# Optimization experiments

Measured on AMD Instinct MI355X. Metric: run time of the kernel, lower is better.

The kernel has to match this reference:

```python
import jax, jax.numpy as jnp
import numpy as np

B, L, D, H = 2, 2048, 1024, 16
DH = D // H
SCALE = DH ** -0.5


def setup_inputs() -> dict:
    key = jax.random.key(0)
    k1, k2, k3 = jax.random.split(key, 3)
    x = jax.random.normal(k1, (B, L, D), dtype=jnp.float32)
    W_qkv = jax.random.normal(k2, (D, 3 * D), dtype=jnp.float32) * 0.02
    b_qkv = jnp.zeros((3 * D,), dtype=jnp.float32)
    W_proj = jax.random.normal(k3, (D, D), dtype=jnp.float32) * 0.02
    b_proj = jnp.zeros((D,), dtype=jnp.float32)
    return {"x": x, "W_qkv": W_qkv, "b_qkv": b_qkv, "W_proj": W_proj, "b_proj": b_proj}


def reference(x, W_qkv, b_qkv, W_proj, b_proj):
    b, l, d = x.shape
    # QKV projection: [B,L,3D] -> [3,B,H,L,DH] matching 'b n (three h d) -> three b h n d'
    qkv = (x @ W_qkv + b_qkv).reshape(b, l, 3, H, DH).transpose(2, 0, 3, 1, 4)
    q, k, v = qkv[0], qkv[1], qkv[2]
    # Causal scores. Chunking in the original is purely a scheduling detail;
    # masks are indexed by absolute row positions, so full attention is identical.
    scores = jnp.einsum('bhqd,bhkd->bhqk', q, k) * SCALE
    mask = jnp.triu(jnp.ones((l, l), dtype=bool), 1)  # True above diagonal
    neg_inf = jnp.finfo(scores.dtype).min
    scores = jnp.where(mask, neg_inf, scores)
    m = jnp.max(scores, axis=-1, keepdims=True)
    e = jnp.where(mask, 0.0, jnp.exp(scores - m))
    attn = e / (jnp.sum(e, axis=-1, keepdims=True) + 1e-6)
    out = jnp.einsum('bhqk,bhkd->bhqd', attn, v)  # [B,H,L,DH]
    out = out.transpose(0, 2, 1, 3).reshape(b, l, d)  # 'b h n d -> b n (h d)'
    return out @ W_proj + b_proj
```

## Files before the change

### kernel.cpp

```cpp
#include <hip/hip_runtime.h>


typedef __bf16 bf16x8 __attribute__((ext_vector_type(8)));
typedef float  f32x4  __attribute__((ext_vector_type(4)));
typedef unsigned short bhalf;
typedef unsigned int   uint32;

#define B_  2
#define L_  2048
#define D_  1024
#define H_  16
#define DH_ 64

#define GPTR(p) ((const __attribute__((address_space(1))) void*)(p))
#define SPTR(p) ((__attribute__((address_space(3))) void*)(p))

static __device__ __forceinline__ float bf2f(bhalf u) {
    union { uint32 u; float f; } x; x.u = ((uint32)u) << 16; return x.f;
}
static __device__ __forceinline__ bhalf f2bf(float f) {
    union { float f; uint32 u; } x; x.f = f;
    uint32 r = x.u + 0x7FFFu + ((x.u >> 16) & 1u);
    return (bhalf)(r >> 16);
}

__global__ void detect_dtype(const uint32* __restrict__ xw, int* __restrict__ flag) {
    int t = threadIdx.x;
    uint32 w = xw[t];
    uint32 e = (w >> 7) & 0xFFu;
    int g = (e < 0x6Fu || e > 0x84u) ? 1 : 0;
#pragma unroll
    for (int off = 32; off; off >>= 1) g += __shfl_xor(g, off);
    if (t == 0) *flag = (g > 16) ? 0 : 1;
}

__global__ void conv_bf16(const void* __restrict__ in, bhalf* __restrict__ out,
                          int n4, const int* __restrict__ flag) {
    const bool isb = (*flag != 0);
    for (int i = blockIdx.x * blockDim.x + threadIdx.x; i < n4;
         i += gridDim.x * blockDim.x) {
        if (isb) {
            ((uint2*)out)[i] = ((const uint2*)in)[i];
        } else {
            float4 v = ((const float4*)in)[i];
            uint2 o;
            o.x = (uint32)f2bf(v.x) | ((uint32)f2bf(v.y) << 16);
            o.y = (uint32)f2bf(v.z) | ((uint32)f2bf(v.w) << 16);
            ((uint2*)out)[i] = o;
        }
    }
}

__global__ void tr_conv(const void* __restrict__ in, bhalf* __restrict__ out,
                        int R, int C, const int* __restrict__ flag) {
    __shared__ bhalf t[32][33];
    const bool isb = (*flag != 0);
    int bx = blockIdx.x, by = blockIdx.y;
    int tx = threadIdx.x, ty = threadIdx.y;
#pragma unroll
    for (int i = 0; i < 32; i += 8) {
        size_t idx = (size_t)(by * 32 + ty + i) * C + bx * 32 + tx;
        t[ty + i][tx] = isb ? ((const bhalf*)in)[idx]
                            : f2bf(((const float*)in)[idx]);
    }
    __syncthreads();
#pragma unroll
    for (int i = 0; i < 32; i += 8)
        out[(size_t)(bx * 32 + ty + i) * R + by * 32 + tx] = t[tx][ty + i];
}


#define GSTAGE(BUF, KK) do {                                                  \
    int kko = (KK);                                                           \
    _Pragma("unroll")                                                         \
    for (int r = 0; r < 2; r++) {                                             \
        int c = r * 256 + tid;                                                \
        int row = c >> 2, p = c & 3;                                          \
        int gch = (p - row - (row >> 2)) & 3;                                 \
        __builtin_amdgcn_global_load_lds(                                     \
            GPTR(a0 + (size_t)row * K + kko + gch * 8),                       \
            SPTR(As[BUF] + (r * 256 + w * 64) * 8), 16, 0, 0);                \
        __builtin_amdgcn_global_load_lds(                                     \
            GPTR(b0 + (size_t)row * K + kko + gch * 8),                       \
            SPTR(Bs[BUF] + (r * 256 + w * 64) * 8), 16, 0, 0);                \
    }                                                                         \
} while (0)

template <int MODE>
__global__ __launch_bounds__(256) void gemm_bt(
        const bhalf* __restrict__ A, const bhalf* __restrict__ Bt,
        const void* __restrict__ bias,
        void* __restrict__ C0, bhalf* __restrict__ Qb,
        bhalf* __restrict__ Kb, bhalf* __restrict__ Vtb,
        int M, int N, int K, const int* __restrict__ flag) {
    __shared__ bhalf As[2][128 * 32];
    __shared__ bhalf Bs[2][128 * 32];
    const bool isb = (*flag != 0);
    const int tid  = threadIdx.x;
    const int w    = tid >> 6, lane = tid & 63;
    const int g    = lane >> 4, cl = lane & 15;
    const int m0   = blockIdx.y * 128, n0 = blockIdx.x * 128;
    const int wr   = (w >> 1) * 64, wc = (w & 1) * 64;

    f32x4 acc[4][4] = {};

    const bhalf* a0 = A  + (size_t)m0 * K;
    const bhalf* b0 = Bt + (size_t)n0 * K;

    GSTAGE(0, 0);
    __syncthreads();

    const int nk = K >> 5;
    for (int t = 0; t < nk; ++t) {
        int cur = t & 1;
        if (t + 1 < nk) GSTAGE(cur ^ 1, (t + 1) << 5);

        bf16x8 af[4], bf4[4];
#pragma unroll
        for (int i = 0; i < 4; i++) {
            int ra = wr + i * 16 + cl;
            af[i]  = *(const bf16x8*)(As[cur] + ra * 32 +
                                      (((g + ra + (ra >> 2)) & 3) * 8));
            int rb = wc + i * 16 + cl;
            bf4[i] = *(const bf16x8*)(Bs[cur] + rb * 32 +
                                      (((g + rb + (rb >> 2)) & 3) * 8));
        }
        __builtin_amdgcn_s_setprio(1);
#pragma unroll
        for (int i = 0; i < 4; i++)
#pragma unroll
            for (int j = 0; j < 4; j++)
                acc[i][j] = __builtin_amdgcn_mfma_f32_16x16x32_bf16(
                    af[i], bf4[j], acc[i][j], 0, 0, 0);
        __builtin_amdgcn_s_setprio(0);

        __syncthreads();
    }

#pragma unroll
    for (int i = 0; i < 4; i++) {
#pragma unroll
        for (int j = 0; j < 4; j++) {
            int nn = n0 + wc + j * 16 + cl;
            float bv = isb ? bf2f(((const bhalf*)bias)[nn])
                           : ((const float*)bias)[nn];
#pragma unroll
            for (int r = 0; r < 4; r++) {
                int mm = m0 + wr + i * 16 + g * 4 + r;
                float v = acc[i][j][r] + bv;
                if (MODE == 0) {
                    if (isb) ((bhalf*)C0)[(size_t)mm * N + nn] = f2bf(v);
                    else     ((float*)C0)[(size_t)mm * N + nn] = v;
                } else {
                    int b = mm >> 11, l = mm & 2047;
                    int three = nn >> 10, rem = nn & 1023;
                    int h = rem >> 6, dh = rem & 63;
                    size_t bh = (size_t)(b * 16 + h);
                    if (three == 0) {
                        Qb[(bh * 2048 + l) * 64 + dh] = f2bf(v * 0.18033688f);
                    } else if (three == 1) {
                        Kb [(bh * 2048 + l) * 64 + dh] = f2bf(v);
                    } else {
                        Vtb[(bh * 64 + dh) * 2048 + l] = f2bf(v);
                    }
                }
            }
        }
    }
}


#define STAGE(BUF, KT) do {                                                   \
    int ktv = (KT);                                                           \
    _Pragma("unroll")                                                         \
    for (int r = 0; r < 4; r++) {                                             \
        int c = r * 256 + tid;                                                \
        int row = c >> 3, p = c & 7;                                          \
        int fsw = (row & 3) | (((row >> 3) & 1) << 2);                        \
        __builtin_amdgcn_global_load_lds(                                     \
            GPTR(Kp + (size_t)(ktv * 128 + row) * 64 + (p ^ fsw) * 8),        \
            SPTR(Ks[BUF] + (r * 256 + w * 64) * 8), 16, 0, 0);                \
    }                                                                         \
    _Pragma("unroll")                                                         \
    for (int r = 0; r < 4; r++) {                                             \
        int c = r * 256 + tid;                                                \
        int row = c >> 4, p = c & 15;                                         \
        __builtin_amdgcn_global_load_lds(                                     \
            GPTR(Vt + (size_t)row * L_ + ktv * 128 + (p ^ (row & 15)) * 8),   \
            SPTR(Vs[BUF] + (r * 256 + w * 64) * 8), 16, 0, 0);                \
    }                                                                         \
} while (0)

#define ATTN_TILE(BUF, KT, QF, QLANE, MVAR, LVAR, OACC, MASK) do {            \
    f32x4 p8[8] = {};                                                         \
    _Pragma("unroll")                                                         \
    for (int s = 0; s < 2; s++) {                                             \
        bf16x8 kf[8];                                                         \
        _Pragma("unroll")                                                     \
        for (int j = 0; j < 8; j++) {                                         \
            int row = (j >> 1) * 32 + (cl >> 2) * 8 + (j & 1) * 4 + (cl & 3); \
            int fsw = (row & 3) | (((row >> 3) & 1) << 2);                    \
            int ch = s * 4 + g;                                               \
            kf[j] = *(const bf16x8*)(Ks[BUF] + row * 64 + ((ch ^ fsw) * 8));  \
        }                                                                     \
        __builtin_amdgcn_s_setprio(1);                                        \
        _Pragma("unroll")                                                     \
        for (int j = 0; j < 8; j++)                                           \
            p8[j] = __builtin_amdgcn_mfma_f32_16x16x32_bf16(                  \
                kf[j], QF[s], p8[j], 0, 0, 0);                                \
        __builtin_amdgcn_s_setprio(0);                                        \
    }                                                                         \
    float mx0 = -__builtin_inff(), mx1 = -__builtin_inff();                   \
    float mx2 = -__builtin_inff(), mx3 = -__builtin_inff();                   \
    _Pragma("unroll")                                                         \
    for (int j = 0; j < 8; j++) {                                             \
        float v0 = p8[j][0], v1 = p8[j][1], v2 = p8[j][2], v3 = p8[j][3];     \
        if (MASK) {                                                           \
            int ka = (KT) * 128 + (j >> 1) * 32 + g * 8 + ((j & 1) << 2);     \
            v0 = (ka + 0 > (QLANE)) ? -__builtin_inff() : v0;                 \
            v1 = (ka + 1 > (QLANE)) ? -__builtin_inff() : v1;                 \
            v2 = (ka + 2 > (QLANE)) ? -__builtin_inff() : v2;                 \
            v3 = (ka + 3 > (QLANE)) ? -__builtin_inff() : v3;                 \
            p8[j][0] = v0; p8[j][1] = v1; p8[j][2] = v2; p8[j][3] = v3;       \
        }                                                                     \
        mx0 = fmaxf(mx0, v0); mx1 = fmaxf(mx1, v1);                           \
        mx2 = fmaxf(mx2, v2); mx3 = fmaxf(mx3, v3);                           \
    }                                                                         \
    float mx = fmaxf(fmaxf(mx0, mx1), fmaxf(mx2, mx3));                       \
    mx = fmaxf(mx, __shfl_xor(mx, 16));                                       \
    mx = fmaxf(mx, __shfl_xor(mx, 32));                                       \
    if (!__all(mx - MVAR <= 8.f)) {       \
        float mnew = fmaxf(MVAR, mx);                                         \
        float alpha = __builtin_amdgcn_exp2f(MVAR - mnew);                    \
        MVAR = mnew;                                                          \
        LVAR *= alpha;                                                        \
        _Pragma("unroll")                                                     \
        for (int r = 0; r < 4; r++) {                                         \
            float ar = __shfl(alpha, g * 4 + r);                              \
            _Pragma("unroll")                                                 \
            for (int dj = 0; dj < 4; dj++) OACC[dj][r] *= ar;                 \
        }                                                                     \
    }                                                                         \
    float s0 = 0.f, s1 = 0.f, s2 = 0.f, s3 = 0.f;                             \
    _Pragma("unroll")                                                         \
    for (int j = 0; j < 8; j++) {                                             \
        float e0 = __builtin_amdgcn_exp2f(p8[j][0] - MVAR);                   \
        float e1 = __builtin_amdgcn_exp2f(p8[j][1] - MVAR);                   \
        float e2 = __builtin_amdgcn_exp2f(p8[j][2] - MVAR);                   \
        float e3 = __builtin_amdgcn_exp2f(p8[j][3] - MVAR);                   \
        p8[j][0] = e0; p8[j][1] = e1; p8[j][2] = e2; p8[j][3] = e3;           \
        s0 += e0; s1 += e1; s2 += e2; s3 += e3;                               \
    }                                                                         \
    float ls = (s0 + s1) + (s2 + s3);                                         \
    ls += __shfl_xor(ls, 16);                                                 \
    ls += __shfl_xor(ls, 32);                                                 \
    LVAR += ls;                                                               \
    _Pragma("unroll")                                                         \
    for (int ks = 0; ks < 4; ks++) {                                          \
        bf16x8 pf;                                                            \
        _Pragma("unroll")                                                     \
        for (int e = 0; e < 8; e++)                                           \
            pf[e] = (__bf16)p8[2 * ks + (e >> 2)][e & 3];                     \
        bf16x8 vf[4];                                                         \
        _Pragma("unroll")                                                     \
        for (int dj = 0; dj < 4; dj++) {                                      \
            int vrow = dj * 16 + cl;                                          \
            int ch = ks * 4 + g;                                              \
            vf[dj] = *(const bf16x8*)(Vs[BUF] + vrow * 128 + ((ch ^ (vrow & 15)) * 8)); \
        }                                                                     \
        __builtin_amdgcn_s_setprio(1);                                        \
        _Pragma("unroll")                                                     \
        for (int dj = 0; dj < 4; dj++)                                        \
            OACC[dj] = __builtin_amdgcn_mfma_f32_16x16x32_bf16(               \
                pf, vf[dj], OACC[dj], 0, 0, 0);                               \
        __builtin_amdgcn_s_setprio(0);                                        \
    }                                                                         \
} while (0)

__global__ __launch_bounds__(256, 2) void attn_fwd(
        const bhalf* __restrict__ Qb, const bhalf* __restrict__ Kb,
        const bhalf* __restrict__ Vtb, bhalf* __restrict__ Ob) {
    __shared__ bhalf Ks[2][128 * 64];
    __shared__ bhalf Vs[2][64 * 128];

    const int bid  = blockIdx.x;
    const int xcd  = bid & 7, slot = bid >> 3;
    const int bx   = slot & 15;
    const int bh   = xcd + 8 * (slot >> 4);
    const int qbA  = 31 - bx;
    const int qbB  = bx;

    const int tid = threadIdx.x;
    const int w = tid >> 6, lane = tid & 63;
    const int g = lane >> 4, cl = lane & 15;

    const bhalf* Q  = Qb  + (size_t)bh * L_ * DH_;
    const bhalf* Kp = Kb  + (size_t)bh * L_ * DH_;
    const bhalf* Vt = Vtb + (size_t)bh * DH_ * L_;

    const int q0A = qbA * 64 + w * 16, qlA = q0A + cl;
    const int q0B = qbB * 64 + w * 16, qlB = q0B + cl;

    bf16x8 qfA[2], qfB[2];
#pragma unroll
    for (int s = 0; s < 2; s++) {
        qfA[s] = *(const bf16x8*)(Q + (size_t)(q0A + cl) * 64 + s * 32 + g * 8);
        qfB[s] = *(const bf16x8*)(Q + (size_t)(q0B + cl) * 64 + s * 32 + g * 8);
    }

    f32x4 oA[4] = {}, oB[4] = {};
    float mA = -__builtin_inff(), lA = 0.f;
    float mB = -__builtin_inff(), lB = 0.f;

    const int nktA = (qbA >> 1) + 1;
    const int nktB = (qbB >> 1) + 1;

    STAGE(0, 0);
    __syncthreads();

    for (int kt = 0; kt < nktA; ++kt) {
        int cur = kt & 1;
        if (kt + 1 < nktA) STAGE(cur ^ 1, kt + 1);
        if (kt < nktB) {
            ATTN_TILE(cur, kt, qfB, qlB, mB, lB, oB, (kt == nktB - 1));
        }
        ATTN_TILE(cur, kt, qfA, qlA, mA, lA, oA, (kt == nktA - 1));
        __syncthreads();
    }

    const int b = bh >> 4, h = bh & 15;
#pragma unroll
    for (int r = 0; r < 4; r++) {
        float lrA = __shfl(lA, g * 4 + r);
        float lrB = __shfl(lB, g * 4 + r);
        float invA = 1.f / (lrA + 1e-6f);
        float invB = 1.f / (lrB + 1e-6f);
        int qrA = q0A + g * 4 + r, qrB = q0B + g * 4 + r;
#pragma unroll
        for (int dj = 0; dj < 4; dj++) {
            Ob[((size_t)b * L_ + qrA) * D_ + h * 64 + dj * 16 + cl] =
                f2bf(oA[dj][r] * invA);
            Ob[((size_t)b * L_ + qrB) * D_ + h * 64 + dj * 16 + cl] =
                f2bf(oB[dj][r] * invB);
        }
    }
}

extern "C" void kernel_launch(void* const* d_in, const int* in_sizes, int n_in,
                              void* d_out, int out_size, void* d_ws, size_t ws_size,
                              hipStream_t stream) {
    const void* x     = d_in[0];
    const void* Wqkv  = d_in[1];
    const void* bqkv  = d_in[2];
    const void* Wproj = d_in[3];
    const void* bproj = d_in[4];

    char* ws = (char*)d_ws;
    const size_t SZ_FLG = 256;
    const size_t SZ_WQT = (size_t)3 * D_ * D_ * 2;
    const size_t SZ_WPT = (size_t)D_ * D_ * 2;
    const size_t SZ_X   = (size_t)B_ * L_ * D_ * 2;
    const size_t SZ_BUF = (size_t)B_ * H_ * L_ * DH_ * 2;

    int*   flag = (int*)ws;
    bhalf* Wq_t = (bhalf*)(ws + SZ_FLG);
    bhalf* Wp_t = (bhalf*)(ws + SZ_FLG + SZ_WQT);
    bhalf* Xb   = (bhalf*)(ws + SZ_FLG + SZ_WQT + SZ_WPT);
    bhalf* Qbuf = (bhalf*)(ws + SZ_FLG + SZ_WQT + SZ_WPT + SZ_X);
    bhalf* Kbuf = (bhalf*)(ws + SZ_FLG + SZ_WQT + SZ_WPT + SZ_X + SZ_BUF);
    bhalf* Vtbf = (bhalf*)(ws + SZ_FLG + SZ_WQT + SZ_WPT + SZ_X + 2 * SZ_BUF);
    bhalf* Obuf = (bhalf*)(ws + SZ_FLG + SZ_WQT + SZ_WPT + SZ_X + 3 * SZ_BUF);

    const int M = B_ * L_;

    detect_dtype<<<1, 64, 0, stream>>>((const uint32*)x, flag);

    conv_bf16<<<2048, 256, 0, stream>>>(x, Xb, (B_ * L_ * D_) / 4, flag);
    tr_conv<<<dim3(3 * D_ / 32, D_ / 32), dim3(32, 8), 0, stream>>>(
        Wqkv, Wq_t, D_, 3 * D_, flag);
    tr_conv<<<dim3(D_ / 32, D_ / 32), dim3(32, 8), 0, stream>>>(
        Wproj, Wp_t, D_, D_, flag);

    gemm_bt<1><<<dim3(3 * D_ / 128, M / 128), 256, 0, stream>>>(
        Xb, Wq_t, bqkv, nullptr, Qbuf, Kbuf, Vtbf, M, 3 * D_, D_, flag);

    attn_fwd<<<dim3(512), 256, 0, stream>>>(Qbuf, Kbuf, Vtbf, Obuf);

    gemm_bt<0><<<dim3(D_ / 128, M / 128), 256, 0, stream>>>(
        Obuf, Wp_t, bproj, d_out, nullptr, nullptr, nullptr, M, D_, D_, flag);
}
```

Before: 125.0 us.

## Triple-buffer GEMM LDS staging and register-stage K/V prefetch in attention

The GEMM moves from double to triple buffering of its LDS tiles. It waits with an explicit vmcnt and uses a single barrier per iteration, so loads run two tiles ahead. The attention kernel drops its double-buffered direct global-to-LDS loads. It now prefetches the next K/V tile into registers and writes them to a single LDS buffer after compute, which halves attention LDS use but adds registers and an extra barrier per tile. In the GEMM, the redundant clamped reload of the last tile on the final iterations and the hand-placed waitcnt both depend on the compiler emitting exactly the expected number of outstanding loads.

```diff
diff --git a/kernel.cpp b/kernel.cpp
--- a/kernel.cpp
+++ b/kernel.cpp
@@ -72,6 +72,7 @@
 
 #define GSTAGE(BUF, KK) do {                                                  \
     int kko = (KK);                                                           \
+    int bufv = (BUF);                                                         \
     _Pragma("unroll")                                                         \
     for (int r = 0; r < 2; r++) {                                             \
         int c = r * 256 + tid;                                                \
@@ -79,10 +80,10 @@
         int gch = (p - row - (row >> 2)) & 3;                                 \
         __builtin_amdgcn_global_load_lds(                                     \
             GPTR(a0 + (size_t)row * K + kko + gch * 8),                       \
-            SPTR(As[BUF] + (r * 256 + w * 64) * 8), 16, 0, 0);                \
+            SPTR(As + bufv * 4096 + (r * 256 + w * 64) * 8), 16, 0, 0);       \
         __builtin_amdgcn_global_load_lds(                                     \
             GPTR(b0 + (size_t)row * K + kko + gch * 8),                       \
-            SPTR(Bs[BUF] + (r * 256 + w * 64) * 8), 16, 0, 0);                \
+            SPTR(Bs + bufv * 4096 + (r * 256 + w * 64) * 8), 16, 0, 0);       \
     }                                                                         \
 } while (0)
 
@@ -93,8 +94,8 @@
         void* __restrict__ C0, bhalf* __restrict__ Qb,
         bhalf* __restrict__ Kb, bhalf* __restrict__ Vtb,
         int M, int N, int K, const int* __restrict__ flag) {
-    __shared__ bhalf As[2][128 * 32];
-    __shared__ bhalf Bs[2][128 * 32];
+    __shared__ bhalf As[3 * 128 * 32];
+    __shared__ bhalf Bs[3 * 128 * 32];
     const bool isb = (*flag != 0);
     const int tid  = threadIdx.x;
     const int w    = tid >> 6, lane = tid & 63;
@@ -107,22 +108,28 @@
     const bhalf* a0 = A  + (size_t)m0 * K;
     const bhalf* b0 = Bt + (size_t)n0 * K;
 
+    const int nk = K >> 5;
     GSTAGE(0, 0);
-    __syncthreads();
-
-    const int nk = K >> 5;
+    GSTAGE(1, 32);
+
     for (int t = 0; t < nk; ++t) {
-        int cur = t & 1;
-        if (t + 1 < nk) GSTAGE(cur ^ 1, (t + 1) << 5);
-
+        asm volatile("s_waitcnt vmcnt(4)" ::: "memory");
+        __builtin_amdgcn_sched_barrier(0);
+        __builtin_amdgcn_s_barrier();
+        __builtin_amdgcn_sched_barrier(0);
+
+        int tp = t + 2 < nk ? t + 2 : nk - 1;
+        GSTAGE((t + 2) % 3, tp << 5);
+
+        int cur = t % 3;
         bf16x8 af[4], bf4[4];
 #pragma unroll
         for (int i = 0; i < 4; i++) {
             int ra = wr + i * 16 + cl;
-            af[i]  = *(const bf16x8*)(As[cur] + ra * 32 +
+            af[i]  = *(const bf16x8*)(As + cur * 4096 + ra * 32 +
                                       (((g + ra + (ra >> 2)) & 3) * 8));
             int rb = wc + i * 16 + cl;
-            bf4[i] = *(const bf16x8*)(Bs[cur] + rb * 32 +
+            bf4[i] = *(const bf16x8*)(Bs + cur * 4096 + rb * 32 +
                                       (((g + rb + (rb >> 2)) & 3) * 8));
         }
         __builtin_amdgcn_s_setprio(1);
@@ -133,8 +140,6 @@
                 acc[i][j] = __builtin_amdgcn_mfma_f32_16x16x32_bf16(
                     af[i], bf4[j], acc[i][j], 0, 0, 0);
         __builtin_amdgcn_s_setprio(0);
-
-        __syncthreads();
     }
 
 #pragma unroll
@@ -170,28 +175,32 @@
 }
 
 
-#define STAGE(BUF, KT) do {                                                   \
+#define KV_ISSUE(KT) do {                                                     \
     int ktv = (KT);                                                           \
     _Pragma("unroll")                                                         \
     for (int r = 0; r < 4; r++) {                                             \
         int c = r * 256 + tid;                                                \
         int row = c >> 3, p = c & 7;                                          \
         int fsw = (row & 3) | (((row >> 3) & 1) << 2);                        \
-        __builtin_amdgcn_global_load_lds(                                     \
-            GPTR(Kp + (size_t)(ktv * 128 + row) * 64 + (p ^ fsw) * 8),        \
-            SPTR(Ks[BUF] + (r * 256 + w * 64) * 8), 16, 0, 0);                \
+        kst[r] = *(const uint4*)(Kp + (size_t)(ktv * 128 + row) * 64 + (p ^ fsw) * 8); \
     }                                                                         \
     _Pragma("unroll")                                                         \
     for (int r = 0; r < 4; r++) {                                             \
         int c = r * 256 + tid;                                                \
         int row = c >> 4, p = c & 15;                                         \
-        __builtin_amdgcn_global_load_lds(                                     \
-            GPTR(Vt + (size_t)row * L_ + ktv * 128 + (p ^ (row & 15)) * 8),   \
-            SPTR(Vs[BUF] + (r * 256 + w * 64) * 8), 16, 0, 0);                \
+        vst[r] = *(const uint4*)(Vt + (size_t)row * L_ + ktv * 128 + (p ^ (row & 15)) * 8); \
     }                                                                         \
 } while (0)
 
-#define ATTN_TILE(BUF, KT, QF, QLANE, MVAR, LVAR, OACC, MASK) do {            \
+#define KV_WRITE() do {                                                       \
+    _Pragma("unroll")                                                         \
+    for (int r = 0; r < 4; r++) {                                             \
+        *(uint4*)(Ks + (r * 256 + tid) * 8) = kst[r];                         \
+        *(uint4*)(Vs + (r * 256 + tid) * 8) = vst[r];                         \
+    }                                                                         \
+} while (0)
+
+#define ATTN_TILE(KT, QF, QLANE, MVAR, LVAR, OACC, MASK) do {                 \
     f32x4 p8[8] = {};                                                         \
     _Pragma("unroll")                                                         \
     for (int s = 0; s < 2; s++) {                                             \
@@ -201,7 +210,7 @@
             int row = (j >> 1) * 32 + (cl >> 2) * 8 + (j & 1) * 4 + (cl & 3); \
             int fsw = (row & 3) | (((row >> 3) & 1) << 2);                    \
             int ch = s * 4 + g;                                               \
-            kf[j] = *(const bf16x8*)(Ks[BUF] + row * 64 + ((ch ^ fsw) * 8));  \
+            kf[j] = *(const bf16x8*)(Ks + row * 64 + ((ch ^ fsw) * 8));       \
         }                                                                     \
         __builtin_amdgcn_s_setprio(1);                                        \
         _Pragma("unroll")                                                     \
@@ -266,7 +275,7 @@
         for (int dj = 0; dj < 4; dj++) {                                      \
             int vrow = dj * 16 + cl;                                          \
             int ch = ks * 4 + g;                                              \
-            vf[dj] = *(const bf16x8*)(Vs[BUF] + vrow * 128 + ((ch ^ (vrow & 15)) * 8)); \
+            vf[dj] = *(const bf16x8*)(Vs + vrow * 128 + ((ch ^ (vrow & 15)) * 8)); \
         }                                                                     \
         __builtin_amdgcn_s_setprio(1);                                        \
         _Pragma("unroll")                                                     \
@@ -280,8 +289,8 @@
 __global__ __launch_bounds__(256, 2) void attn_fwd(
         const bhalf* __restrict__ Qb, const bhalf* __restrict__ Kb,
         const bhalf* __restrict__ Vtb, bhalf* __restrict__ Ob) {
-    __shared__ bhalf Ks[2][128 * 64];
-    __shared__ bhalf Vs[2][64 * 128];
+    __shared__ bhalf Ks[128 * 64];
+    __shared__ bhalf Vs[64 * 128];
 
     const int bid  = blockIdx.x;
     const int xcd  = bid & 7, slot = bid >> 3;
@@ -315,17 +324,23 @@
     const int nktA = (qbA >> 1) + 1;
     const int nktB = (qbB >> 1) + 1;
 
-    STAGE(0, 0);
+    uint4 kst[4], vst[4];
+
+    KV_ISSUE(0);
+    KV_WRITE();
     __syncthreads();
 
     for (int kt = 0; kt < nktA; ++kt) {
-        int cur = kt & 1;
-        if (kt + 1 < nktA) STAGE(cur ^ 1, kt + 1);
+        if (kt + 1 < nktA) KV_ISSUE(kt + 1);
         if (kt < nktB) {
-            ATTN_TILE(cur, kt, qfB, qlB, mB, lB, oB, (kt == nktB - 1));
-        }
-        ATTN_TILE(cur, kt, qfA, qlA, mA, lA, oA, (kt == nktA - 1));
+            ATTN_TILE(kt, qfB, qlB, mB, lB, oB, (kt == nktB - 1));
+        }
+        ATTN_TILE(kt, qfA, qlA, mA, lA, oA, (kt == nktA - 1));
         __syncthreads();
+        if (kt + 1 < nktA) {
+            KV_WRITE();
+            __syncthreads();
+        }
     }
 
     const int b = bh >> 4, h = bh & 15;
```

Result: slower. 171.3 us (+37.1%).

## Split paired-query attention blocks into single-block CTAs with 64-key tiles

Applied to the files above, without the earlier changes.

The attention kernel drops the pairing of a long and a short causal query block per workgroup. Each workgroup now handles one 64-row query block and walks the keys in 64-wide tiles instead of 128-wide ones, and the grid doubles to 1024 blocks. LDS use is halved and launch bounds rise to 4 blocks per CU, aiming for more occupancy and finer causal masking. The cost is that K/V tiles are no longer shared between two query blocks, there are more sync iterations, and per-block work becomes uneven.

```diff
diff --git a/kernel.cpp b/kernel.cpp
--- a/kernel.cpp
+++ b/kernel.cpp
@@ -173,31 +173,31 @@
 #define STAGE(BUF, KT) do {                                                   \
     int ktv = (KT);                                                           \
     _Pragma("unroll")                                                         \
-    for (int r = 0; r < 4; r++) {                                             \
+    for (int r = 0; r < 2; r++) {                                             \
         int c = r * 256 + tid;                                                \
         int row = c >> 3, p = c & 7;                                          \
         int fsw = (row & 3) | (((row >> 3) & 1) << 2);                        \
         __builtin_amdgcn_global_load_lds(                                     \
-            GPTR(Kp + (size_t)(ktv * 128 + row) * 64 + (p ^ fsw) * 8),        \
+            GPTR(Kp + (size_t)(ktv * 64 + row) * 64 + (p ^ fsw) * 8),         \
             SPTR(Ks[BUF] + (r * 256 + w * 64) * 8), 16, 0, 0);                \
     }                                                                         \
     _Pragma("unroll")                                                         \
-    for (int r = 0; r < 4; r++) {                                             \
+    for (int r = 0; r < 2; r++) {                                             \
         int c = r * 256 + tid;                                                \
-        int row = c >> 4, p = c & 15;                                         \
+        int row = c >> 3, p = c & 7;                                          \
         __builtin_amdgcn_global_load_lds(                                     \
-            GPTR(Vt + (size_t)row * L_ + ktv * 128 + (p ^ (row & 15)) * 8),   \
+            GPTR(Vt + (size_t)row * L_ + ktv * 64 + (p ^ (row & 7)) * 8),     \
             SPTR(Vs[BUF] + (r * 256 + w * 64) * 8), 16, 0, 0);                \
     }                                                                         \
 } while (0)
 
 #define ATTN_TILE(BUF, KT, QF, QLANE, MVAR, LVAR, OACC, MASK) do {            \
-    f32x4 p8[8] = {};                                                         \
+    f32x4 p8[4] = {};                                                         \
     _Pragma("unroll")                                                         \
     for (int s = 0; s < 2; s++) {                                             \
-        bf16x8 kf[8];                                                         \
-        _Pragma("unroll")                                                     \
-        for (int j = 0; j < 8; j++) {                                         \
+        bf16x8 kf[4];                                                         \
+        _Pragma("unroll")                                                     \
+        for (int j = 0; j < 4; j++) {                                         \
             int row = (j >> 1) * 32 + (cl >> 2) * 8 + (j & 1) * 4 + (cl & 3); \
             int fsw = (row & 3) | (((row >> 3) & 1) << 2);                    \
             int ch = s * 4 + g;                                               \
@@ -205,7 +205,7 @@
         }                                                                     \
         __builtin_amdgcn_s_setprio(1);                                        \
         _Pragma("unroll")                                                     \
-        for (int j = 0; j < 8; j++)                                           \
+        for (int j = 0; j < 4; j++)                                           \
             p8[j] = __builtin_amdgcn_mfma_f32_16x16x32_bf16(                  \
                 kf[j], QF[s], p8[j], 0, 0, 0);                                \
         __builtin_amdgcn_s_setprio(0);                                        \
@@ -213,10 +213,10 @@
     float mx0 = -__builtin_inff(), mx1 = -__builtin_inff();                   \
     float mx2 = -__builtin_inff(), mx3 = -__builtin_inff();                   \
     _Pragma("unroll")                                                         \
-    for (int j = 0; j < 8; j++) {                                             \
+    for (int j = 0; j < 4; j++) {                                             \
         float v0 = p8[j][0], v1 = p8[j][1], v2 = p8[j][2], v3 = p8[j][3];     \
         if (MASK) {                                                           \
-            int ka = (KT) * 128 + (j >> 1) * 32 + g * 8 + ((j & 1) << 2);     \
+            int ka = (KT) * 64 + (j >> 1) * 32 + g * 8 + ((j & 1) << 2);      \
             v0 = (ka + 0 > (QLANE)) ? -__builtin_inff() : v0;                 \
             v1 = (ka + 1 > (QLANE)) ? -__builtin_inff() : v1;                 \
             v2 = (ka + 2 > (QLANE)) ? -__builtin_inff() : v2;                 \
@@ -229,7 +229,7 @@
     float mx = fmaxf(fmaxf(mx0, mx1), fmaxf(mx2, mx3));                       \
     mx = fmaxf(mx, __shfl_xor(mx, 16));                                       \
     mx = fmaxf(mx, __shfl_xor(mx, 32));                                       \
-    if (!__all(mx - MVAR <= 8.f)) {       \
+    if (!__all(mx - MVAR <= 8.f)) {                            \
         float mnew = fmaxf(MVAR, mx);                                         \
         float alpha = __builtin_amdgcn_exp2f(MVAR - mnew);                    \
         MVAR = mnew;                                                          \
@@ -243,7 +243,7 @@
     }                                                                         \
     float s0 = 0.f, s1 = 0.f, s2 = 0.f, s3 = 0.f;                             \
     _Pragma("unroll")                                                         \
-    for (int j = 0; j < 8; j++) {                                             \
+    for (int j = 0; j < 4; j++) {                                             \
         float e0 = __builtin_amdgcn_exp2f(p8[j][0] - MVAR);                   \
         float e1 = __builtin_amdgcn_exp2f(p8[j][1] - MVAR);                   \
         float e2 = __builtin_amdgcn_exp2f(p8[j][2] - MVAR);                   \
@@ -256,7 +256,7 @@
     ls += __shfl_xor(ls, 32);                                                 \
     LVAR += ls;                                                               \
     _Pragma("unroll")                                                         \
-    for (int ks = 0; ks < 4; ks++) {                                          \
+    for (int ks = 0; ks < 2; ks++) {                                          \
         bf16x8 pf;                                                            \
         _Pragma("unroll")                                                     \
         for (int e = 0; e < 8; e++)                                           \
@@ -266,7 +266,7 @@
         for (int dj = 0; dj < 4; dj++) {                                      \
             int vrow = dj * 16 + cl;                                          \
             int ch = ks * 4 + g;                                              \
-            vf[dj] = *(const bf16x8*)(Vs[BUF] + vrow * 128 + ((ch ^ (vrow & 15)) * 8)); \
+            vf[dj] = *(const bf16x8*)(Vs[BUF] + vrow * 64 + ((ch ^ (vrow & 7)) * 8)); \
         }                                                                     \
         __builtin_amdgcn_s_setprio(1);                                        \
         _Pragma("unroll")                                                     \
@@ -277,18 +277,17 @@
     }                                                                         \
 } while (0)
 
-__global__ __launch_bounds__(256, 2) void attn_fwd(
+__global__ __launch_bounds__(256, 4) void attn_fwd(
         const bhalf* __restrict__ Qb, const bhalf* __restrict__ Kb,
         const bhalf* __restrict__ Vtb, bhalf* __restrict__ Ob) {
-    __shared__ bhalf Ks[2][128 * 64];
-    __shared__ bhalf Vs[2][64 * 128];
+    __shared__ bhalf Ks[2][64 * 64];
+    __shared__ bhalf Vs[2][64 * 64];
 
     const int bid  = blockIdx.x;
     const int xcd  = bid & 7, slot = bid >> 3;
-    const int bx   = slot & 15;
-    const int bh   = xcd + 8 * (slot >> 4);
-    const int qbA  = 31 - bx;
-    const int qbB  = bx;
+    const int v    = slot & 31, grp = slot >> 5;
+    const int qb   = (grp & 1) ? v : (31 - v);
+    const int bh   = xcd + 8 * grp;
 
     const int tid = threadIdx.x;
     const int w = tid >> 6, lane = tid & 63;
@@ -298,51 +297,39 @@
     const bhalf* Kp = Kb  + (size_t)bh * L_ * DH_;
     const bhalf* Vt = Vtb + (size_t)bh * DH_ * L_;
 
-    const int q0A = qbA * 64 + w * 16, qlA = q0A + cl;
-    const int q0B = qbB * 64 + w * 16, qlB = q0B + cl;
-
-    bf16x8 qfA[2], qfB[2];
-#pragma unroll
-    for (int s = 0; s < 2; s++) {
-        qfA[s] = *(const bf16x8*)(Q + (size_t)(q0A + cl) * 64 + s * 32 + g * 8);
-        qfB[s] = *(const bf16x8*)(Q + (size_t)(q0B + cl) * 64 + s * 32 + g * 8);
-    }
-
-    f32x4 oA[4] = {}, oB[4] = {};
-    float mA = -__builtin_inff(), lA = 0.f;
-    float mB = -__builtin_inff(), lB = 0.f;
-
-    const int nktA = (qbA >> 1) + 1;
-    const int nktB = (qbB >> 1) + 1;
+    const int q0 = qb * 64 + w * 16;
+    const int ql = q0 + cl;
+
+    bf16x8 qf[2];
+#pragma unroll
+    for (int s = 0; s < 2; s++)
+        qf[s] = *(const bf16x8*)(Q + (size_t)(q0 + cl) * 64 + s * 32 + g * 8);
+
+    f32x4 oacc[4] = {};
+    float m = -__builtin_inff(), l = 0.f;
+
+    const int nkt = qb + 1;
 
     STAGE(0, 0);
     __syncthreads();
 
-    for (int kt = 0; kt < nktA; ++kt) {
+    for (int kt = 0; kt < nkt; ++kt) {
         int cur = kt & 1;
-        if (kt + 1 < nktA) STAGE(cur ^ 1, kt + 1);
-        if (kt < nktB) {
-            ATTN_TILE(cur, kt, qfB, qlB, mB, lB, oB, (kt == nktB - 1));
-        }
-        ATTN_TILE(cur, kt, qfA, qlA, mA, lA, oA, (kt == nktA - 1));
+        if (kt + 1 < nkt) STAGE(cur ^ 1, kt + 1);
+        ATTN_TILE(cur, kt, qf, ql, m, l, oacc, (kt == nkt - 1));
         __syncthreads();
     }
 
     const int b = bh >> 4, h = bh & 15;
 #pragma unroll
     for (int r = 0; r < 4; r++) {
-        float lrA = __shfl(lA, g * 4 + r);
-        float lrB = __shfl(lB, g * 4 + r);
-        float invA = 1.f / (lrA + 1e-6f);
-        float invB = 1.f / (lrB + 1e-6f);
-        int qrA = q0A + g * 4 + r, qrB = q0B + g * 4 + r;
-#pragma unroll
-        for (int dj = 0; dj < 4; dj++) {
-            Ob[((size_t)b * L_ + qrA) * D_ + h * 64 + dj * 16 + cl] =
-                f2bf(oA[dj][r] * invA);
-            Ob[((size_t)b * L_ + qrB) * D_ + h * 64 + dj * 16 + cl] =
-                f2bf(oB[dj][r] * invB);
-        }
+        float lr  = __shfl(l, g * 4 + r);
+        float inv = 1.f / (lr + 1e-6f);
+        int qrow = q0 + g * 4 + r;
+#pragma unroll
+        for (int dj = 0; dj < 4; dj++)
+            Ob[((size_t)b * L_ + qrow) * D_ + h * 64 + dj * 16 + cl] =
+                f2bf(oacc[dj][r] * inv);
     }
 }
 
@@ -384,7 +371,7 @@
     gemm_bt<1><<<dim3(3 * D_ / 128, M / 128), 256, 0, stream>>>(
         Xb, Wq_t, bqkv, nullptr, Qbuf, Kbuf, Vtbf, M, 3 * D_, D_, flag);
 
-    attn_fwd<<<dim3(512), 256, 0, stream>>>(Qbuf, Kbuf, Vtbf, Obuf);
+    attn_fwd<<<dim3(1024), 256, 0, stream>>>(Qbuf, Kbuf, Vtbf, Obuf);
 
     gemm_bt<0><<<dim3(D_ / 128, M / 128), 256, 0, stream>>>(
         Obuf, Wp_t, bproj, d_out, nullptr, nullptr, nullptr, M, D_, D_, flag);
```

Result: slower. 129.6 us (+3.7%).

## Fuse fp32-to-bf16 input conversion into QKV GEMM and drop dtype detection

Applied to the files above, without the earlier changes.

The QKV GEMM now stages fp32 activations straight into LDS with an 8-chunk swizzle and converts them to bf16 in registers before the MFMA. This removes the separate conversion kernel and its bf16 copy of x. The runtime dtype-detection kernel and its flag branches are also dropped, hardcoding fp32 inputs and outputs. In exchange the A tile takes twice the LDS and global traffic per k-step, plus conversion ALU work inside the main loop.

```diff
diff --git a/kernel.cpp b/kernel.cpp
--- a/kernel.cpp
+++ b/kernel.cpp
@@ -24,78 +24,30 @@
     return (bhalf)(r >> 16);
 }
 
-__global__ void detect_dtype(const uint32* __restrict__ xw, int* __restrict__ flag) {
-    int t = threadIdx.x;
-    uint32 w = xw[t];
-    uint32 e = (w >> 7) & 0xFFu;
-    int g = (e < 0x6Fu || e > 0x84u) ? 1 : 0;
-#pragma unroll
-    for (int off = 32; off; off >>= 1) g += __shfl_xor(g, off);
-    if (t == 0) *flag = (g > 16) ? 0 : 1;
-}
-
-__global__ void conv_bf16(const void* __restrict__ in, bhalf* __restrict__ out,
-                          int n4, const int* __restrict__ flag) {
-    const bool isb = (*flag != 0);
-    for (int i = blockIdx.x * blockDim.x + threadIdx.x; i < n4;
-         i += gridDim.x * blockDim.x) {
-        if (isb) {
-            ((uint2*)out)[i] = ((const uint2*)in)[i];
-        } else {
-            float4 v = ((const float4*)in)[i];
-            uint2 o;
-            o.x = (uint32)f2bf(v.x) | ((uint32)f2bf(v.y) << 16);
-            o.y = (uint32)f2bf(v.z) | ((uint32)f2bf(v.w) << 16);
-            ((uint2*)out)[i] = o;
-        }
-    }
-}
-
-__global__ void tr_conv(const void* __restrict__ in, bhalf* __restrict__ out,
-                        int R, int C, const int* __restrict__ flag) {
+__global__ void tr_conv(const float* __restrict__ in, bhalf* __restrict__ out,
+                        int R, int C) {
     __shared__ bhalf t[32][33];
-    const bool isb = (*flag != 0);
     int bx = blockIdx.x, by = blockIdx.y;
     int tx = threadIdx.x, ty = threadIdx.y;
 #pragma unroll
-    for (int i = 0; i < 32; i += 8) {
-        size_t idx = (size_t)(by * 32 + ty + i) * C + bx * 32 + tx;
-        t[ty + i][tx] = isb ? ((const bhalf*)in)[idx]
-                            : f2bf(((const float*)in)[idx]);
-    }
+    for (int i = 0; i < 32; i += 8)
+        t[ty + i][tx] = f2bf(in[(size_t)(by * 32 + ty + i) * C + bx * 32 + tx]);
     __syncthreads();
 #pragma unroll
     for (int i = 0; i < 32; i += 8)
         out[(size_t)(bx * 32 + ty + i) * R + by * 32 + tx] = t[tx][ty + i];
 }
 
-
-#define GSTAGE(BUF, KK) do {                                                  \
-    int kko = (KK);                                                           \
-    _Pragma("unroll")                                                         \
-    for (int r = 0; r < 2; r++) {                                             \
-        int c = r * 256 + tid;                                                \
-        int row = c >> 2, p = c & 3;                                          \
-        int gch = (p - row - (row >> 2)) & 3;                                 \
-        __builtin_amdgcn_global_load_lds(                                     \
-            GPTR(a0 + (size_t)row * K + kko + gch * 8),                       \
-            SPTR(As[BUF] + (r * 256 + w * 64) * 8), 16, 0, 0);                \
-        __builtin_amdgcn_global_load_lds(                                     \
-            GPTR(b0 + (size_t)row * K + kko + gch * 8),                       \
-            SPTR(Bs[BUF] + (r * 256 + w * 64) * 8), 16, 0, 0);                \
-    }                                                                         \
-} while (0)
-
 template <int MODE>
 __global__ __launch_bounds__(256) void gemm_bt(
-        const bhalf* __restrict__ A, const bhalf* __restrict__ Bt,
-        const void* __restrict__ bias,
-        void* __restrict__ C0, bhalf* __restrict__ Qb,
+        const void* __restrict__ A, const bhalf* __restrict__ Bt,
+        const float* __restrict__ bias,
+        float* __restrict__ C0, bhalf* __restrict__ Qb,
         bhalf* __restrict__ Kb, bhalf* __restrict__ Vtb,
-        int M, int N, int K, const int* __restrict__ flag) {
-    __shared__ bhalf As[2][128 * 32];
-    __shared__ bhalf Bs[2][128 * 32];
-    const bool isb = (*flag != 0);
+        int M, int N, int K) {
+    __shared__ float AsF[(MODE == 1) ? 2 * 128 * 32 : 2];
+    __shared__ bhalf AsH[(MODE == 0) ? 2 * 128 * 32 : 2];
+    __shared__ bhalf Bs[2 * 128 * 32];
     const int tid  = threadIdx.x;
     const int w    = tid >> 6, lane = tid & 63;
     const int g    = lane >> 4, cl = lane & 15;
@@ -104,25 +56,70 @@
 
     f32x4 acc[4][4] = {};
 
-    const bhalf* a0 = A  + (size_t)m0 * K;
-    const bhalf* b0 = Bt + (size_t)n0 * K;
-
-    GSTAGE(0, 0);
+    const float* a0f = (const float*)A + (size_t)m0 * K;
+    const bhalf* a0h = (const bhalf*)A + (size_t)m0 * K;
+    const bhalf* b0  = Bt + (size_t)n0 * K;
+
+    auto stage = [&](int buf, int kk) {
+        if (MODE == 1) {
+#pragma unroll
+            for (int r = 0; r < 4; r++) {
+                int c = r * 256 + tid;
+                int row = c >> 3, p = c & 7;
+                int gch = (p - row) & 7;
+                __builtin_amdgcn_global_load_lds(
+                    GPTR(a0f + (size_t)row * K + kk + gch * 4),
+                    SPTR(AsF + buf * 4096 + (r * 256 + w * 64) * 4), 16, 0, 0);
+            }
+        } else {
+#pragma unroll
+            for (int r = 0; r < 2; r++) {
+                int c = r * 256 + tid;
+                int row = c >> 2, p = c & 3;
+                int gch = (p - row - (row >> 2)) & 3;
+                __builtin_amdgcn_global_load_lds(
+                    GPTR(a0h + (size_t)row * K + kk + gch * 8),
+                    SPTR(AsH + buf * 4096 + (r * 256 + w * 64) * 8), 16, 0, 0);
+            }
+        }
+#pragma unroll
+        for (int r = 0; r < 2; r++) {
+            int c = r * 256 + tid;
+            int row = c >> 2, p = c & 3;
+            int gch = (p - row - (row >> 2)) & 3;
+            __builtin_amdgcn_global_load_lds(
+                GPTR(b0 + (size_t)row * K + kk + gch * 8),
+                SPTR(Bs + buf * 4096 + (r * 256 + w * 64) * 8), 16, 0, 0);
+        }
+    };
+
+    stage(0, 0);
     __syncthreads();
 
     const int nk = K >> 5;
     for (int t = 0; t < nk; ++t) {
         int cur = t & 1;
-        if (t + 1 < nk) GSTAGE(cur ^ 1, (t + 1) << 5);
+        if (t + 1 < nk) stage(cur ^ 1, (t + 1) << 5);
 
         bf16x8 af[4], bf4[4];
 #pragma unroll
         for (int i = 0; i < 4; i++) {
             int ra = wr + i * 16 + cl;
-            af[i]  = *(const bf16x8*)(As[cur] + ra * 32 +
-                                      (((g + ra + (ra >> 2)) & 3) * 8));
+            if (MODE == 1) {
+                const float* base = AsF + cur * 4096 + ra * 32;
+                f32x4 x0 = *(const f32x4*)(base + (((2 * g + ra) & 7) * 4));
+                f32x4 x1 = *(const f32x4*)(base + (((2 * g + 1 + ra) & 7) * 4));
+#pragma unroll
+                for (int e = 0; e < 4; e++) {
+                    af[i][e]     = (__bf16)x0[e];
+                    af[i][4 + e] = (__bf16)x1[e];
+                }
+            } else {
+                af[i] = *(const bf16x8*)(AsH + cur * 4096 + ra * 32 +
+                                         (((g + ra + (ra >> 2)) & 3) * 8));
+            }
             int rb = wc + i * 16 + cl;
-            bf4[i] = *(const bf16x8*)(Bs[cur] + rb * 32 +
+            bf4[i] = *(const bf16x8*)(Bs + cur * 4096 + rb * 32 +
                                       (((g + rb + (rb >> 2)) & 3) * 8));
         }
         __builtin_amdgcn_s_setprio(1);
@@ -142,15 +139,13 @@
 #pragma unroll
         for (int j = 0; j < 4; j++) {
             int nn = n0 + wc + j * 16 + cl;
-            float bv = isb ? bf2f(((const bhalf*)bias)[nn])
-                           : ((const float*)bias)[nn];
+            float bv = bias[nn];
 #pragma unroll
             for (int r = 0; r < 4; r++) {
                 int mm = m0 + wr + i * 16 + g * 4 + r;
                 float v = acc[i][j][r] + bv;
                 if (MODE == 0) {
-                    if (isb) ((bhalf*)C0)[(size_t)mm * N + nn] = f2bf(v);
-                    else     ((float*)C0)[(size_t)mm * N + nn] = v;
+                    C0[(size_t)mm * N + nn] = v;
                 } else {
                     int b = mm >> 11, l = mm & 2047;
                     int three = nn >> 10, rem = nn & 1023;
@@ -229,7 +224,7 @@
     float mx = fmaxf(fmaxf(mx0, mx1), fmaxf(mx2, mx3));                       \
     mx = fmaxf(mx, __shfl_xor(mx, 16));                                       \
     mx = fmaxf(mx, __shfl_xor(mx, 32));                                       \
-    if (!__all(mx - MVAR <= 8.f)) {       \
+    if (!__all(mx - MVAR <= 8.f)) {                            \
         float mnew = fmaxf(MVAR, mx);                                         \
         float alpha = __builtin_amdgcn_exp2f(MVAR - mnew);                    \
         MVAR = mnew;                                                          \
@@ -349,43 +344,36 @@
 extern "C" void kernel_launch(void* const* d_in, const int* in_sizes, int n_in,
                               void* d_out, int out_size, void* d_ws, size_t ws_size,
                               hipStream_t stream) {
-    const void* x     = d_in[0];
-    const void* Wqkv  = d_in[1];
-    const void* bqkv  = d_in[2];
-    const void* Wproj = d_in[3];
-    const void* bproj = d_in[4];
+    const float* x     = (const float*)d_in[0];
+    const float* Wqkv  = (const float*)d_in[1];
+    const float* bqkv  = (const float*)d_in[2];
+    const float* Wproj = (const float*)d_in[3];
+    const float* bproj = (const float*)d_in[4];
 
     char* ws = (char*)d_ws;
-    const size_t SZ_FLG = 256;
     const size_t SZ_WQT = (size_t)3 * D_ * D_ * 2;
     const size_t SZ_WPT = (size_t)D_ * D_ * 2;
-    const size_t SZ_X   = (size_t)B_ * L_ * D_ * 2;
     const size_t SZ_BUF = (size_t)B_ * H_ * L_ * DH_ * 2;
 
-    int*   flag = (int*)ws;
-    bhalf* Wq_t = (bhalf*)(ws + SZ_FLG);
-    bhalf* Wp_t = (bhalf*)(ws + SZ_FLG + SZ_WQT);
-    bhalf* Xb   = (bhalf*)(ws + SZ_FLG + SZ_WQT + SZ_WPT);
-    bhalf* Qbuf = (bhalf*)(ws + SZ_FLG + SZ_WQT + SZ_WPT + SZ_X);
-    bhalf* Kbuf = (bhalf*)(ws + SZ_FLG + SZ_WQT + SZ_WPT + SZ_X + SZ_BUF);
-    bhalf* Vtbf = (bhalf*)(ws + SZ_FLG + SZ_WQT + SZ_WPT + SZ_X + 2 * SZ_BUF);
-    bhalf* Obuf = (bhalf*)(ws + SZ_FLG + SZ_WQT + SZ_WPT + SZ_X + 3 * SZ_BUF);
+    bhalf* Wq_t = (bhalf*)(ws);
+    bhalf* Wp_t = (bhalf*)(ws + SZ_WQT);
+    bhalf* Qbuf = (bhalf*)(ws + SZ_WQT + SZ_WPT);
+    bhalf* Kbuf = (bhalf*)(ws + SZ_WQT + SZ_WPT + SZ_BUF);
+    bhalf* Vtbf = (bhalf*)(ws + SZ_WQT + SZ_WPT + 2 * SZ_BUF);
+    bhalf* Obuf = (bhalf*)(ws + SZ_WQT + SZ_WPT + 3 * SZ_BUF);
 
     const int M = B_ * L_;
 
-    detect_dtype<<<1, 64, 0, stream>>>((const uint32*)x, flag);
-
-    conv_bf16<<<2048, 256, 0, stream>>>(x, Xb, (B_ * L_ * D_) / 4, flag);
     tr_conv<<<dim3(3 * D_ / 32, D_ / 32), dim3(32, 8), 0, stream>>>(
-        Wqkv, Wq_t, D_, 3 * D_, flag);
+        Wqkv, Wq_t, D_, 3 * D_);
     tr_conv<<<dim3(D_ / 32, D_ / 32), dim3(32, 8), 0, stream>>>(
-        Wproj, Wp_t, D_, D_, flag);
+        Wproj, Wp_t, D_, D_);
 
     gemm_bt<1><<<dim3(3 * D_ / 128, M / 128), 256, 0, stream>>>(
-        Xb, Wq_t, bqkv, nullptr, Qbuf, Kbuf, Vtbf, M, 3 * D_, D_, flag);
+        x, Wq_t, bqkv, nullptr, Qbuf, Kbuf, Vtbf, M, 3 * D_, D_);
 
     attn_fwd<<<dim3(512), 256, 0, stream>>>(Qbuf, Kbuf, Vtbf, Obuf);
 
     gemm_bt<0><<<dim3(D_ / 128, M / 128), 256, 0, stream>>>(
-        Obuf, Wp_t, bproj, d_out, nullptr, nullptr, nullptr, M, D_, D_, flag);
-}
+        Obuf, Wp_t, bproj, (float*)d_out, nullptr, nullptr, nullptr, M, D_, D_);
+}
```

After: 118.6 us. -5.2%, faster.
